# Performance work log

Hardware: AMD Instinct MI355X
Metric: run time of the kernel (lower is better)

The kernel has to match this reference:

```python
import jax, jax.numpy as jnp
import numpy as np

B, C_IN, H, W = 4, 256, 48, 48
HEADS, HD = 8, 64
N = H * W
SCALE = 1.0 / (HD ** 0.5)


def setup_inputs() -> dict:
    key = jax.random.key(0)
    ks = jax.random.split(key, 5)
    x = jax.random.normal(ks[0], (B, C_IN, H, W), dtype=jnp.float32)
    # 1x1 conv weights, squeezed: [heads, head_channels, in_channels]
    Wq = jax.random.normal(ks[1], (HEADS, HD, C_IN), dtype=jnp.float32) * (C_IN ** -0.5)
    Wk = jax.random.normal(ks[2], (HEADS, HD, C_IN), dtype=jnp.float32) * (C_IN ** -0.5)
    Wv = jax.random.normal(ks[3], (HEADS, HD, C_IN), dtype=jnp.float32) * (C_IN ** -0.5)
    # output 1x1 conv: [in_channels, heads*head_channels]
    Wo = jax.random.normal(ks[4], (C_IN, HEADS * HD), dtype=jnp.float32) * ((HEADS * HD) ** -0.5)
    return {"x": x, "Wq": Wq, "Wk": Wk, "Wv": Wv, "Wo": Wo}


def reference(x, Wq, Wk, Wv, Wo):
    b, c, h, w = x.shape
    n = h * w
    xf = x.reshape(b, c, n)  # [B, C, N]
    # per-head 1x1 convs == batched projections -> [heads, B, N, HD]
    q = jnp.einsum('hdc,bcn->hbnd', Wq, xf)
    k = jnp.einsum('hdc,bcn->hbnd', Wk, xf)
    v = jnp.einsum('hdc,bcn->hbnd', Wv, xf)
    scores = jnp.einsum('hbnd,hbmd->hbnm', q, k) * SCALE  # [heads, B, N, N]
    probs = jax.nn.softmax(scores, axis=-1)
    ws = jnp.einsum('hbnm,hbmd->hbnd', probs, v)  # [heads, B, N, HD]
    # faithful replication of torch: transpose(1,2) then reshape(B, heads*HD, H, W)
    ws = jnp.transpose(ws, (0, 2, 1, 3))  # [heads, N, B, HD]
    ws = ws.reshape(b, HEADS * HD, h, w)
    out = jnp.einsum('oc,bchw->bohw', Wo, ws)  # output 1x1 conv
    return out
```

## Files before the change

kernel.cpp:

```cpp
#include <hip/hip_runtime.h>

#define B_     4
#define CIN    256
#define NTOK   2304
#define HEADS  8
#define HD     64
#define SCALE  0.125f
#define LOG2E  1.44269504088896f
#define QSCALE (SCALE * LOG2E)
#define PBIAS  4.0f
#define QKV_ELEMS (HEADS * B_ * NTOK * HD)
#define HBSTRIDE 147456
#define WSZ    131072

typedef _Float16 f16;
typedef _Float16 __attribute__((ext_vector_type(8))) h8v;
typedef _Float16 __attribute__((ext_vector_type(4))) h4v;
typedef ushort   __attribute__((ext_vector_type(8))) us8;
typedef float    __attribute__((ext_vector_type(16))) f16v;

__device__ inline uint pk2(float a, float b) {
    auto v = __builtin_amdgcn_cvt_pkrtz(a, b);
    return __builtin_bit_cast(uint, v);
}
#define EXP2(x) __builtin_amdgcn_exp2f(x)

#define GLOAD_LDS(g, l) __builtin_amdgcn_global_load_lds( \
    (const __attribute__((address_space(1))) unsigned int*)(g), \
    (__attribute__((address_space(3))) unsigned int*)(l), 16, 0, 0)

__global__ __launch_bounds__(256) void castw(
    const float* __restrict__ Wq, const float* __restrict__ Wk,
    const float* __restrict__ Wv, const float* __restrict__ Wo,
    f16* __restrict__ wc, f16* __restrict__ woc)
{
    int e4 = (blockIdx.x * 256 + threadIdx.x) * 4;
    const float* src; f16* dst; float mult = 1.0f; int off;
    if (e4 < WSZ)          { src = Wq; off = e4;           dst = wc;           mult = QSCALE; }
    else if (e4 < 2 * WSZ) { src = Wk; off = e4 - WSZ;     dst = wc + WSZ; }
    else if (e4 < 3 * WSZ) { src = Wv; off = e4 - 2 * WSZ; dst = wc + 2 * WSZ; }
    else                   { src = Wo; off = e4 - 3 * WSZ; dst = woc; }
    float4 r = *(const float4*)(src + off);
    h4v hv;
    hv.x = (f16)(r.x * mult); hv.y = (f16)(r.y * mult);
    hv.z = (f16)(r.z * mult); hv.w = (f16)(r.w * mult);
    *(h4v*)(dst + off) = hv;
}

__global__ __launch_bounds__(256) void tcastf(
    const float* __restrict__ src, f16* __restrict__ dst, int C)
{
    const int n0 = blockIdx.x * 64;
    const int c0 = blockIdx.y * 64;
    const int b  = blockIdx.z;
    __shared__ float T[64][65];
    const int tid = threadIdx.x;
    const float* sb = src + ((size_t)b * C + c0) * NTOK;
    #pragma unroll
    for (int i = 0; i < 16; ++i) {
        int idx = tid + 256 * i;
        int rr = idx >> 6, ll = idx & 63;
        T[ll][rr] = sb[(size_t)rr * NTOK + n0 + ll];
    }
    __syncthreads();
    const size_t ob = ((size_t)b * NTOK + n0) * C + c0;
    #pragma unroll
    for (int i = 0; i < 4; ++i) {
        int idx = tid + 256 * i;
        int row = idx >> 4, c4 = (idx & 15) * 4;
        h4v v;
        v.x = (f16)T[row][c4 + 0]; v.y = (f16)T[row][c4 + 1];
        v.z = (f16)T[row][c4 + 2]; v.w = (f16)T[row][c4 + 3];
        *(h4v*)(dst + ob + (size_t)row * C + c4) = v;
    }
}

__global__ __launch_bounds__(128) void proj_mfma(
    const f16* __restrict__ wc, const f16* __restrict__ xt,
    f16* __restrict__ qh, f16* __restrict__ kh, f16* __restrict__ vth)
{
    const int ntile = blockIdx.x;
    const int hp    = blockIdx.y;
    const int b     = blockIdx.z;
    const int p     = hp >> 3, h = hp & 7;
    const int hb    = h * 4 + b;
    const f16* Wp = wc + ((size_t)p * 8 + h) * (HD * CIN);

    __shared__ __align__(16) f16 Ws[2][64][64], Xs[2][64][64];

    const int tid = threadIdx.x;
    const int w = tid >> 6, lane = tid & 63;
    const int lm = lane & 31, lh = lane >> 5;
    const int n_loc  = w * 32 + lm;
    const int n_glob = ntile * 64 + n_loc;

    const f16* xb = xt + ((size_t)b * NTOK + ntile * 64) * CIN;

    auto stage = [&](int buf, int c0) {
        const f16* src = (w == 0) ? Wp : xb;
        f16* dst = (w == 0) ? &Ws[buf][0][0] : &Xs[buf][0][0];
        #pragma unroll
        for (int i = 0; i < 8; ++i) {
            int g = i * 64 + lane; int row = g >> 3; int c = (g & 7) ^ (row & 7);
            GLOAD_LDS(src + (size_t)row * CIN + c0 + c * 8, dst + i * 512);
        }
    };

    f16v o0, o1;
    #pragma unroll
    for (int i = 0; i < 16; ++i) { o0[i] = 0.f; o1[i] = 0.f; }

    stage(0, 0);
    for (int c0 = 0; c0 < CIN; c0 += 64) {
        const int cur = (c0 >> 6) & 1;
        __syncthreads();
        if (c0 + 64 < CIN) stage(cur ^ 1, c0 + 64);
        #pragma unroll
        for (int s = 0; s < 4; ++s) {
            const int pp = ((2 * s + lh) ^ (lm & 7)) * 8;
            h8v a0 = *(const h8v*)&Ws[cur][lm][pp];
            h8v a1 = *(const h8v*)&Ws[cur][lm + 32][pp];
            h8v bh = *(const h8v*)&Xs[cur][n_loc][pp];
            o0 = __builtin_amdgcn_mfma_f32_32x32x16_f16(a0, bh, o0, 0, 0, 0);
            o1 = __builtin_amdgcn_mfma_f32_32x32x16_f16(a1, bh, o1, 0, 0, 0);
        }
    }

    const size_t hboff = (size_t)hb * HBSTRIDE;
    if (p < 2) {
        f16* oh = ((p == 0) ? qh : kh) + hboff + (size_t)n_glob * 64;
        #pragma unroll
        for (int t = 0; t < 2; ++t) {
            const f16v& oc = t ? o1 : o0;
            #pragma unroll
            for (int g = 0; g < 4; ++g) {
                int d0 = 8 * g + 4 * lh + 32 * t;
                h4v hv;
                hv.x = (f16)oc[4 * g + 0]; hv.y = (f16)oc[4 * g + 1];
                hv.z = (f16)oc[4 * g + 2]; hv.w = (f16)oc[4 * g + 3];
                *(h4v*)(oh + d0) = hv;
            }
        }
    } else {
        f16* oh = vth + hboff;
        #pragma unroll
        for (int t = 0; t < 2; ++t) {
            const f16v& oc = t ? o1 : o0;
            #pragma unroll
            for (int r = 0; r < 16; ++r) {
                int d = (r & 3) + 8 * (r >> 2) + 4 * lh + 32 * t;
                oh[(size_t)d * NTOK + n_glob] = (f16)oc[r];
            }
        }
    }
}

__global__ __launch_bounds__(256, 2) void attn_mfma(
    const f16* __restrict__ qh, const f16* __restrict__ kh,
    const f16* __restrict__ vth, f16* __restrict__ wsth)
{
    const int bid   = blockIdx.x;
    const int xcd   = bid & 7;
    const int slot  = bid >> 3;
    const int hb    = xcd * 4 + (slot / 18);
    const int rpair = slot % 18;
    const int h_    = hb >> 2, b = hb & 3;
    const int tid   = threadIdx.x;
    const int w     = tid >> 6;
    const int lane  = tid & 63;
    const int lm    = lane & 31;
    const int lh    = lane >> 5;
    const int qg    = w >> 1;
    const int ks    = w & 1;

    __shared__ __align__(16) f16 SMEM[2][2][2][64][64];

    const size_t hboff = (size_t)hb * HBSTRIDE;
    const int mA = rpair * 128 + qg * 64 + lm;
    const int mB = mA + 32;

    h8v QfA[4], QfB[4];
    #pragma unroll
    for (int s = 0; s < 4; ++s) {
        QfA[s] = *(const h8v*)(qh + hboff + (size_t)mA * 64 + (2 * s + lh) * 8);
        QfB[s] = *(const h8v*)(qh + hboff + (size_t)mB * 64 + (2 * s + lh) * 8);
    }

    f16v oA0, oA1, oB0, oB1;
    #pragma unroll
    for (int i = 0; i < 16; ++i) { oA0[i] = 0.f; oA1[i] = 0.f; oB0[i] = 0.f; oB1[i] = 0.f; }
    float lsumA = 0.f, lsumB = 0.f;

    const int  sv  = w >> 1;
    const int  stp = w & 1;
    const f16* gb  = (sv == 0) ? kh + hboff : vth + hboff;

    auto stage = [&](int buf, int st) {
        const int kts = 2 * st + stp;
        f16* dst = &SMEM[buf][sv][stp][0][0];
        #pragma unroll
        for (int i = 0; i < 8; ++i) {
            int g   = i * 64 + lane;
            int row = g >> 3;
            int c   = (g & 7) ^ (row & 7);
            const f16* src = (sv == 0)
                ? gb + kts * 4096 + row * 64 + c * 8
                : gb + (size_t)row * 2304 + kts * 64 + c * 8;
            GLOAD_LDS(src, dst + i * 512);
        }
    };

    stage(0, 0);
    __syncthreads();

    for (int st = 0; st < 18; ++st) {
        const int cur = st & 1;
        if (st + 1 < 18) stage(cur ^ 1, st + 1);

        f16v sA0, sA1, sB0, sB1;
        #pragma unroll
        for (int i = 0; i < 16; ++i) {
            sA0[i] = -PBIAS; sA1[i] = -PBIAS; sB0[i] = -PBIAS; sB1[i] = -PBIAS;
        }

        __builtin_amdgcn_s_setprio(1);
        #pragma unroll
        for (int s = 0; s < 4; ++s) {
            const int p = ((2 * s + lh) ^ (lm & 7)) * 8;
            h8v k0 = *(const h8v*)&SMEM[cur][0][ks][lm][p];
            h8v k1 = *(const h8v*)&SMEM[cur][0][ks][lm + 32][p];
            sA0 = __builtin_amdgcn_mfma_f32_32x32x16_f16(k0, QfA[s], sA0, 0, 0, 0);
            sA1 = __builtin_amdgcn_mfma_f32_32x32x16_f16(k1, QfA[s], sA1, 0, 0, 0);
            sB0 = __builtin_amdgcn_mfma_f32_32x32x16_f16(k0, QfB[s], sB0, 0, 0, 0);
            sB1 = __builtin_amdgcn_mfma_f32_32x32x16_f16(k1, QfB[s], sB1, 0, 0, 0);
        }
        __builtin_amdgcn_s_setprio(0);

        float rsA = 0.f, rsB = 0.f;
        #pragma unroll
        for (int i = 0; i < 16; ++i) { sA0[i] = EXP2(sA0[i]); rsA += sA0[i]; }
        #pragma unroll
        for (int i = 0; i < 16; ++i) { sA1[i] = EXP2(sA1[i]); rsA += sA1[i]; }
        #pragma unroll
        for (int i = 0; i < 16; ++i) { sB0[i] = EXP2(sB0[i]); rsB += sB0[i]; }
        #pragma unroll
        for (int i = 0; i < 16; ++i) { sB1[i] = EXP2(sB1[i]); rsB += sB1[i]; }
        lsumA += rsA; lsumB += rsB;

        uint PpkA[2][8], PpkB[2][8];
        #pragma unroll
        for (int pr = 0; pr < 8; ++pr) {
            PpkA[0][pr] = pk2(sA0[2 * pr], sA0[2 * pr + 1]);
            PpkA[1][pr] = pk2(sA1[2 * pr], sA1[2 * pr + 1]);
            PpkB[0][pr] = pk2(sB0[2 * pr], sB0[2 * pr + 1]);
            PpkB[1][pr] = pk2(sB1[2 * pr], sB1[2 * pr + 1]);
        }

        h8v pfA[4], pfB[4];
        #pragma unroll
        for (int s = 0; s < 4; ++s) {
            const int jt = s >> 1, q = 4 * (s & 1);
            auto a02 = __builtin_amdgcn_permlane32_swap(
                PpkA[jt][q + 0], PpkA[jt][q + 2], false, false);
            auto a13 = __builtin_amdgcn_permlane32_swap(
                PpkA[jt][q + 1], PpkA[jt][q + 3], false, false);
            uint4 ua = { a02[0], a13[0], a02[1], a13[1] };
            pfA[s] = __builtin_bit_cast(h8v, ua);
            auto b02 = __builtin_amdgcn_permlane32_swap(
                PpkB[jt][q + 0], PpkB[jt][q + 2], false, false);
            auto b13 = __builtin_amdgcn_permlane32_swap(
                PpkB[jt][q + 1], PpkB[jt][q + 3], false, false);
            uint4 ub = { b02[0], b13[0], b02[1], b13[1] };
            pfB[s] = __builtin_bit_cast(h8v, ub);
        }

        __builtin_amdgcn_s_setprio(1);
        #pragma unroll
        for (int s = 0; s < 4; ++s) {
            const int p = ((2 * s + lh) ^ (lm & 7)) * 8;
            h8v v0 = *(const h8v*)&SMEM[cur][1][ks][lm][p];
            h8v v1 = *(const h8v*)&SMEM[cur][1][ks][lm + 32][p];
            oA0 = __builtin_amdgcn_mfma_f32_32x32x16_f16(v0, pfA[s], oA0, 0, 0, 0);
            oA1 = __builtin_amdgcn_mfma_f32_32x32x16_f16(v1, pfA[s], oA1, 0, 0, 0);
            oB0 = __builtin_amdgcn_mfma_f32_32x32x16_f16(v0, pfB[s], oB0, 0, 0, 0);
            oB1 = __builtin_amdgcn_mfma_f32_32x32x16_f16(v1, pfB[s], oB1, 0, 0, 0);
        }
        __builtin_amdgcn_s_setprio(0);

        __syncthreads();
    }

    float* red = (float*)&SMEM[0][0][0][0][0];
    if (ks == 1) {
        float* dA = red + (size_t)(qg * 128 + lane) * 33;
        float* dB = red + (size_t)(qg * 128 + 64 + lane) * 33;
        #pragma unroll
        for (int i = 0; i < 16; ++i) {
            dA[i] = oA0[i]; dA[16 + i] = oA1[i];
            dB[i] = oB0[i]; dB[16 + i] = oB1[i];
        }
        dA[32] = lsumA; dB[32] = lsumB;
    }
    __syncthreads();
    if (ks == 0) {
        const float* sA = red + (size_t)(qg * 128 + lane) * 33;
        const float* sB = red + (size_t)(qg * 128 + 64 + lane) * 33;
        #pragma unroll
        for (int i = 0; i < 16; ++i) {
            oA0[i] += sA[i]; oA1[i] += sA[16 + i];
            oB0[i] += sB[i]; oB1[i] += sB[16 + i];
        }
        lsumA += sA[32]; lsumB += sB[32];
        lsumA += __shfl_xor(lsumA, 32);
        lsumB += __shfl_xor(lsumB, 32);
        float invA = 1.0f / lsumA, invB = 1.0f / lsumB;

        f16* wrA = wsth + ((size_t)h_ * NTOK + mA) * 256 + b * 64;
        f16* wrB = wsth + ((size_t)h_ * NTOK + mB) * 256 + b * 64;
        #pragma unroll
        for (int g = 0; g < 4; ++g) {
            h4v r0, r1;
            r0.x = (f16)(oA0[4 * g + 0] * invA); r0.y = (f16)(oA0[4 * g + 1] * invA);
            r0.z = (f16)(oA0[4 * g + 2] * invA); r0.w = (f16)(oA0[4 * g + 3] * invA);
            *(h4v*)(wrA + 8 * g + 4 * lh) = r0;
            r1.x = (f16)(oA1[4 * g + 0] * invA); r1.y = (f16)(oA1[4 * g + 1] * invA);
            r1.z = (f16)(oA1[4 * g + 2] * invA); r1.w = (f16)(oA1[4 * g + 3] * invA);
            *(h4v*)(wrA + 32 + 8 * g + 4 * lh) = r1;
        }
        #pragma unroll
        for (int g = 0; g < 4; ++g) {
            h4v r0, r1;
            r0.x = (f16)(oB0[4 * g + 0] * invB); r0.y = (f16)(oB0[4 * g + 1] * invB);
            r0.z = (f16)(oB0[4 * g + 2] * invB); r0.w = (f16)(oB0[4 * g + 3] * invB);
            *(h4v*)(wrB + 8 * g + 4 * lh) = r0;
            r1.x = (f16)(oB1[4 * g + 0] * invB); r1.y = (f16)(oB1[4 * g + 1] * invB);
            r1.z = (f16)(oB1[4 * g + 2] * invB); r1.w = (f16)(oB1[4 * g + 3] * invB);
            *(h4v*)(wrB + 32 + 8 * g + 4 * lh) = r1;
        }
    }
}

__global__ __launch_bounds__(128) void outconv_mfma(
    const f16* __restrict__ woc, const f16* __restrict__ ws,
    float* __restrict__ out)
{
    const int ntile = blockIdx.x;
    const int otile = blockIdx.y;
    const int b     = blockIdx.z;

    __shared__ __align__(16) f16 Wos[2][64][64];
    __shared__ __align__(16) f16 Xs[2][64][72];

    const int tid = threadIdx.x;
    const int w = tid >> 6, lane = tid & 63;
    const int lm = lane & 31, lh = lane >> 5;
    const int n_loc  = w * 32 + lm;
    const int n_glob = ntile * 64 + n_loc;
    const int pr = tid >> 2;
    const int qn = tid & 3;

    const f16* Wb = woc + (size_t)(otile * 64) * 512;
    const f16* wsb = ws + (size_t)b * 512 * NTOK + ntile * 64 + qn * 16;

    auto stageW = [&](int buf, int c0) {
        #pragma unroll
        for (int j = 0; j < 4; ++j) {
            int i = w * 4 + j;
            int g = i * 64 + lane; int row = g >> 3; int c = (g & 7) ^ (row & 7);
            GLOAD_LDS(Wb + (size_t)row * 512 + c0 + c * 8,
                      &Wos[buf][0][0] + i * 512);
        }
    };

    uint4 x0, x1, x2, x3;
    auto loadB = [&](int c0) {
        const f16* r0 = wsb + (size_t)(c0 + 2 * pr) * NTOK;
        const f16* r1 = r0 + NTOK;
        x0 = *(const uint4*)(r0);
        x1 = *(const uint4*)(r0 + 8);
        x2 = *(const uint4*)(r1);
        x3 = *(const uint4*)(r1 + 8);
    };
    auto storeB = [&](int buf) {
        us8 a0 = __builtin_bit_cast(us8, x0), a1 = __builtin_bit_cast(us8, x1);
        us8 b0 = __builtin_bit_cast(us8, x2), b1 = __builtin_bit_cast(us8, x3);
        #pragma unroll
        for (int j = 0; j < 8; ++j) {
            *(uint*)&Xs[buf][qn * 16 + j][2 * pr]     = (uint)a0[j] | ((uint)b0[j] << 16);
            *(uint*)&Xs[buf][qn * 16 + 8 + j][2 * pr] = (uint)a1[j] | ((uint)b1[j] << 16);
        }
    };

    f16v o0, o1;
    #pragma unroll
    for (int i = 0; i < 16; ++i) { o0[i] = 0.f; o1[i] = 0.f; }

    stageW(0, 0);
    loadB(0);
    storeB(0);
    for (int c0 = 0; c0 < 512; c0 += 64) {
        const int cur = (c0 >> 6) & 1;
        __syncthreads();
        if (c0 + 64 < 512) { stageW(cur ^ 1, c0 + 64); loadB(c0 + 64); }
        #pragma unroll
        for (int s = 0; s < 4; ++s) {
            const int pp = ((2 * s + lh) ^ (lm & 7)) * 8;
            const int co = (2 * s + lh) * 8;
            h8v a0 = *(const h8v*)&Wos[cur][lm][pp];
            h8v a1 = *(const h8v*)&Wos[cur][lm + 32][pp];
            h8v bh = *(const h8v*)&Xs[cur][n_loc][co];
            o0 = __builtin_amdgcn_mfma_f32_32x32x16_f16(a0, bh, o0, 0, 0, 0);
            o1 = __builtin_amdgcn_mfma_f32_32x32x16_f16(a1, bh, o1, 0, 0, 0);
        }
        if (c0 + 64 < 512) storeB(cur ^ 1);
    }

    #pragma unroll
    for (int t = 0; t < 2; ++t) {
        const f16v& oc = t ? o1 : o0;
        #pragma unroll
        for (int r = 0; r < 16; ++r) {
            int orow = otile * 64 + (r & 3) + 8 * (r >> 2) + 4 * lh + 32 * t;
            out[((size_t)b * CIN + orow) * NTOK + n_glob] = oc[r];
        }
    }
}

extern "C" void kernel_launch(void* const* d_in, const int* in_sizes, int n_in,
                              void* d_out, int out_size, void* d_ws, size_t ws_size,
                              hipStream_t stream)
{
    const float* x  = (const float*)d_in[0];
    const float* Wq = (const float*)d_in[1];
    const float* Wk = (const float*)d_in[2];
    const float* Wv = (const float*)d_in[3];
    const float* Wo = (const float*)d_in[4];
    float* out = (float*)d_out;

    f16* qh   = (f16*)d_ws;
    f16* kh   = qh   + QKV_ELEMS;
    f16* vth  = kh   + QKV_ELEMS;
    f16* wsth = vth  + QKV_ELEMS;
    f16* xt   = wsth;
    f16* wc   = wsth + QKV_ELEMS;
    f16* woc  = wc   + 3 * WSZ;

    castw<<<dim3(512), 256, 0, stream>>>(Wq, Wk, Wv, Wo, wc, woc);
    tcastf<<<dim3(36, 4, 4), 256, 0, stream>>>(x, xt, CIN);
    proj_mfma<<<dim3(36, 24, 4), 128, 0, stream>>>(wc, xt, qh, kh, vth);
    attn_mfma<<<dim3(576), 256, 0, stream>>>(qh, kh, vth, wsth);
    outconv_mfma<<<dim3(36, 4, 4), 128, 0, stream>>>(woc, wsth, out);
}
```

Baseline: 172.6 us.

## Drop key-split in attention and merge weight/input cast kernels into one launch

The attention kernel previously used four waves per block, two query groups times two key splits, and reduced partial outputs through LDS at the end. It now uses two waves per block, each owning a 64-row query tile and walking all 36 key tiles, with one wave staging K and the other V. This removes the cross-wave reduction and halves LDS per block. The cost is half as many waves per block and a longer serial loop per wave, which may reduce latency hiding. Separately, the weight-cast and input-transpose kernels are fused into one launch to save a kernel dispatch.

```diff
diff --git a/kernel.cpp b/kernel.cpp
--- a/kernel.cpp
+++ b/kernel.cpp
@@ -29,33 +29,36 @@
     (const __attribute__((address_space(1))) unsigned int*)(g), \
     (__attribute__((address_space(3))) unsigned int*)(l), 16, 0, 0)
 
-__global__ __launch_bounds__(256) void castw(
+__global__ __launch_bounds__(256) void prep(
+    const float* __restrict__ x,
     const float* __restrict__ Wq, const float* __restrict__ Wk,
     const float* __restrict__ Wv, const float* __restrict__ Wo,
-    f16* __restrict__ wc, f16* __restrict__ woc)
+    f16* __restrict__ wc, f16* __restrict__ woc, f16* __restrict__ xt)
 {
-    int e4 = (blockIdx.x * 256 + threadIdx.x) * 4;
-    const float* src; f16* dst; float mult = 1.0f; int off;
-    if (e4 < WSZ)          { src = Wq; off = e4;           dst = wc;           mult = QSCALE; }
-    else if (e4 < 2 * WSZ) { src = Wk; off = e4 - WSZ;     dst = wc + WSZ; }
-    else if (e4 < 3 * WSZ) { src = Wv; off = e4 - 2 * WSZ; dst = wc + 2 * WSZ; }
-    else                   { src = Wo; off = e4 - 3 * WSZ; dst = woc; }
-    float4 r = *(const float4*)(src + off);
-    h4v hv;
-    hv.x = (f16)(r.x * mult); hv.y = (f16)(r.y * mult);
-    hv.z = (f16)(r.z * mult); hv.w = (f16)(r.w * mult);
-    *(h4v*)(dst + off) = hv;
-}
-
-__global__ __launch_bounds__(256) void tcastf(
-    const float* __restrict__ src, f16* __restrict__ dst, int C)
-{
-    const int n0 = blockIdx.x * 64;
-    const int c0 = blockIdx.y * 64;
-    const int b  = blockIdx.z;
     __shared__ float T[64][65];
+    const int bid = blockIdx.x;
     const int tid = threadIdx.x;
-    const float* sb = src + ((size_t)b * C + c0) * NTOK;
+
+    if (bid < 512) {
+        int e4 = (bid * 256 + tid) * 4;
+        const float* src; f16* dst; float mult = 1.0f; int off;
+        if (e4 < WSZ)          { src = Wq; off = e4;           dst = wc;           mult = QSCALE; }
+        else if (e4 < 2 * WSZ) { src = Wk; off = e4 - WSZ;     dst = wc + WSZ; }
+        else if (e4 < 3 * WSZ) { src = Wv; off = e4 - 2 * WSZ; dst = wc + 2 * WSZ; }
+        else                   { src = Wo; off = e4 - 3 * WSZ; dst = woc; }
+        float4 r = *(const float4*)(src + off);
+        h4v hv;
+        hv.x = (f16)(r.x * mult); hv.y = (f16)(r.y * mult);
+        hv.z = (f16)(r.z * mult); hv.w = (f16)(r.w * mult);
+        *(h4v*)(dst + off) = hv;
+        return;
+    }
+
+    const int r  = bid - 512;
+    const int n0 = (r % 36) * 64;
+    const int c0 = ((r / 36) % 4) * 64;
+    const int b  = r / 144;
+    const float* sb = x + ((size_t)b * CIN + c0) * NTOK;
     #pragma unroll
     for (int i = 0; i < 16; ++i) {
         int idx = tid + 256 * i;
@@ -63,7 +66,7 @@
         T[ll][rr] = sb[(size_t)rr * NTOK + n0 + ll];
     }
     __syncthreads();
-    const size_t ob = ((size_t)b * NTOK + n0) * C + c0;
+    const size_t ob = ((size_t)b * NTOK + n0) * CIN + c0;
     #pragma unroll
     for (int i = 0; i < 4; ++i) {
         int idx = tid + 256 * i;
@@ -71,7 +74,7 @@
         h4v v;
         v.x = (f16)T[row][c4 + 0]; v.y = (f16)T[row][c4 + 1];
         v.z = (f16)T[row][c4 + 2]; v.w = (f16)T[row][c4 + 3];
-        *(h4v*)(dst + ob + (size_t)row * C + c4) = v;
+        *(h4v*)(xt + ob + (size_t)row * CIN + c4) = v;
     }
 }
 
@@ -155,7 +158,7 @@
     }
 }
 
-__global__ __launch_bounds__(256, 2) void attn_mfma(
+__global__ __launch_bounds__(128, 2) void attn_mfma(
     const f16* __restrict__ qh, const f16* __restrict__ kh,
     const f16* __restrict__ vth, f16* __restrict__ wsth)
 {
@@ -163,20 +166,18 @@
     const int xcd   = bid & 7;
     const int slot  = bid >> 3;
     const int hb    = xcd * 4 + (slot / 18);
-    const int rpair = slot % 18;
+    const int rtile = slot % 18;
     const int h_    = hb >> 2, b = hb & 3;
     const int tid   = threadIdx.x;
     const int w     = tid >> 6;
     const int lane  = tid & 63;
     const int lm    = lane & 31;
     const int lh    = lane >> 5;
-    const int qg    = w >> 1;
-    const int ks    = w & 1;
-
-    __shared__ __align__(16) f16 SMEM[2][2][2][64][64];
+
+    __shared__ __align__(16) f16 SMEM[2][2][64][64];
 
     const size_t hboff = (size_t)hb * HBSTRIDE;
-    const int mA = rpair * 128 + qg * 64 + lm;
+    const int mA = rtile * 128 + w * 64 + lm;
     const int mB = mA + 32;
 
     h8v QfA[4], QfB[4];
@@ -191,21 +192,18 @@
     for (int i = 0; i < 16; ++i) { oA0[i] = 0.f; oA1[i] = 0.f; oB0[i] = 0.f; oB1[i] = 0.f; }
     float lsumA = 0.f, lsumB = 0.f;
 
-    const int  sv  = w >> 1;
-    const int  stp = w & 1;
-    const f16* gb  = (sv == 0) ? kh + hboff : vth + hboff;
-
-    auto stage = [&](int buf, int st) {
-        const int kts = 2 * st + stp;
-        f16* dst = &SMEM[buf][sv][stp][0][0];
+    const f16* gb = (w == 0) ? kh + hboff : vth + hboff;
+
+    auto stage = [&](int buf, int kt) {
+        f16* dst = &SMEM[buf][w][0][0];
         #pragma unroll
         for (int i = 0; i < 8; ++i) {
             int g   = i * 64 + lane;
             int row = g >> 3;
             int c   = (g & 7) ^ (row & 7);
-            const f16* src = (sv == 0)
-                ? gb + kts * 4096 + row * 64 + c * 8
-                : gb + (size_t)row * 2304 + kts * 64 + c * 8;
+            const f16* src = (w == 0)
+                ? gb + kt * 4096 + row * 64 + c * 8
+                : gb + (size_t)row * 2304 + kt * 64 + c * 8;
             GLOAD_LDS(src, dst + i * 512);
         }
     };
@@ -213,9 +211,9 @@
     stage(0, 0);
     __syncthreads();
 
-    for (int st = 0; st < 18; ++st) {
-        const int cur = st & 1;
-        if (st + 1 < 18) stage(cur ^ 1, st + 1);
+    for (int kt = 0; kt < 36; ++kt) {
+        const int cur = kt & 1;
+        if (kt + 1 < 36) stage(cur ^ 1, kt + 1);
 
         f16v sA0, sA1, sB0, sB1;
         #pragma unroll
@@ -227,8 +225,8 @@
         #pragma unroll
         for (int s = 0; s < 4; ++s) {
             const int p = ((2 * s + lh) ^ (lm & 7)) * 8;
-            h8v k0 = *(const h8v*)&SMEM[cur][0][ks][lm][p];
-            h8v k1 = *(const h8v*)&SMEM[cur][0][ks][lm + 32][p];
+            h8v k0 = *(const h8v*)&SMEM[cur][0][lm][p];
+            h8v k1 = *(const h8v*)&SMEM[cur][0][lm + 32][p];
             sA0 = __builtin_amdgcn_mfma_f32_32x32x16_f16(k0, QfA[s], sA0, 0, 0, 0);
             sA1 = __builtin_amdgcn_mfma_f32_32x32x16_f16(k1, QfA[s], sA1, 0, 0, 0);
             sB0 = __builtin_amdgcn_mfma_f32_32x32x16_f16(k0, QfB[s], sB0, 0, 0, 0);
@@ -278,8 +276,8 @@
         #pragma unroll
         for (int s = 0; s < 4; ++s) {
             const int p = ((2 * s + lh) ^ (lm & 7)) * 8;
-            h8v v0 = *(const h8v*)&SMEM[cur][1][ks][lm][p];
-            h8v v1 = *(const h8v*)&SMEM[cur][1][ks][lm + 32][p];
+            h8v v0 = *(const h8v*)&SMEM[cur][1][lm][p];
+            h8v v1 = *(const h8v*)&SMEM[cur][1][lm + 32][p];
             oA0 = __builtin_amdgcn_mfma_f32_32x32x16_f16(v0, pfA[s], oA0, 0, 0, 0);
             oA1 = __builtin_amdgcn_mfma_f32_32x32x16_f16(v1, pfA[s], oA1, 0, 0, 0);
             oB0 = __builtin_amdgcn_mfma_f32_32x32x16_f16(v0, pfB[s], oB0, 0, 0, 0);
@@ -290,53 +288,31 @@
         __syncthreads();
     }
 
-    float* red = (float*)&SMEM[0][0][0][0][0];
-    if (ks == 1) {
-        float* dA = red + (size_t)(qg * 128 + lane) * 33;
-        float* dB = red + (size_t)(qg * 128 + 64 + lane) * 33;
-        #pragma unroll
-        for (int i = 0; i < 16; ++i) {
-            dA[i] = oA0[i]; dA[16 + i] = oA1[i];
-            dB[i] = oB0[i]; dB[16 + i] = oB1[i];
-        }
-        dA[32] = lsumA; dB[32] = lsumB;
-    }
-    __syncthreads();
-    if (ks == 0) {
-        const float* sA = red + (size_t)(qg * 128 + lane) * 33;
-        const float* sB = red + (size_t)(qg * 128 + 64 + lane) * 33;
-        #pragma unroll
-        for (int i = 0; i < 16; ++i) {
-            oA0[i] += sA[i]; oA1[i] += sA[16 + i];
-            oB0[i] += sB[i]; oB1[i] += sB[16 + i];
-        }
-        lsumA += sA[32]; lsumB += sB[32];
-        lsumA += __shfl_xor(lsumA, 32);
-        lsumB += __shfl_xor(lsumB, 32);
-        float invA = 1.0f / lsumA, invB = 1.0f / lsumB;
-
-        f16* wrA = wsth + ((size_t)h_ * NTOK + mA) * 256 + b * 64;
-        f16* wrB = wsth + ((size_t)h_ * NTOK + mB) * 256 + b * 64;
-        #pragma unroll
-        for (int g = 0; g < 4; ++g) {
-            h4v r0, r1;
-            r0.x = (f16)(oA0[4 * g + 0] * invA); r0.y = (f16)(oA0[4 * g + 1] * invA);
-            r0.z = (f16)(oA0[4 * g + 2] * invA); r0.w = (f16)(oA0[4 * g + 3] * invA);
-            *(h4v*)(wrA + 8 * g + 4 * lh) = r0;
-            r1.x = (f16)(oA1[4 * g + 0] * invA); r1.y = (f16)(oA1[4 * g + 1] * invA);
-            r1.z = (f16)(oA1[4 * g + 2] * invA); r1.w = (f16)(oA1[4 * g + 3] * invA);
-            *(h4v*)(wrA + 32 + 8 * g + 4 * lh) = r1;
-        }
-        #pragma unroll
-        for (int g = 0; g < 4; ++g) {
-            h4v r0, r1;
-            r0.x = (f16)(oB0[4 * g + 0] * invB); r0.y = (f16)(oB0[4 * g + 1] * invB);
-            r0.z = (f16)(oB0[4 * g + 2] * invB); r0.w = (f16)(oB0[4 * g + 3] * invB);
-            *(h4v*)(wrB + 8 * g + 4 * lh) = r0;
-            r1.x = (f16)(oB1[4 * g + 0] * invB); r1.y = (f16)(oB1[4 * g + 1] * invB);
-            r1.z = (f16)(oB1[4 * g + 2] * invB); r1.w = (f16)(oB1[4 * g + 3] * invB);
-            *(h4v*)(wrB + 32 + 8 * g + 4 * lh) = r1;
-        }
+    lsumA += __shfl_xor(lsumA, 32);
+    lsumB += __shfl_xor(lsumB, 32);
+    float invA = 1.0f / lsumA, invB = 1.0f / lsumB;
+
+    f16* wrA = wsth + ((size_t)h_ * NTOK + mA) * 256 + b * 64;
+    f16* wrB = wsth + ((size_t)h_ * NTOK + mB) * 256 + b * 64;
+    #pragma unroll
+    for (int g = 0; g < 4; ++g) {
+        h4v r0, r1;
+        r0.x = (f16)(oA0[4 * g + 0] * invA); r0.y = (f16)(oA0[4 * g + 1] * invA);
+        r0.z = (f16)(oA0[4 * g + 2] * invA); r0.w = (f16)(oA0[4 * g + 3] * invA);
+        *(h4v*)(wrA + 8 * g + 4 * lh) = r0;
+        r1.x = (f16)(oA1[4 * g + 0] * invA); r1.y = (f16)(oA1[4 * g + 1] * invA);
+        r1.z = (f16)(oA1[4 * g + 2] * invA); r1.w = (f16)(oA1[4 * g + 3] * invA);
+        *(h4v*)(wrA + 32 + 8 * g + 4 * lh) = r1;
+    }
+    #pragma unroll
+    for (int g = 0; g < 4; ++g) {
+        h4v r0, r1;
+        r0.x = (f16)(oB0[4 * g + 0] * invB); r0.y = (f16)(oB0[4 * g + 1] * invB);
+        r0.z = (f16)(oB0[4 * g + 2] * invB); r0.w = (f16)(oB0[4 * g + 3] * invB);
+        *(h4v*)(wrB + 8 * g + 4 * lh) = r0;
+        r1.x = (f16)(oB1[4 * g + 0] * invB); r1.y = (f16)(oB1[4 * g + 1] * invB);
+        r1.z = (f16)(oB1[4 * g + 2] * invB); r1.w = (f16)(oB1[4 * g + 3] * invB);
+        *(h4v*)(wrB + 32 + 8 * g + 4 * lh) = r1;
     }
 }
 
@@ -445,9 +421,8 @@
     f16* wc   = wsth + QKV_ELEMS;
     f16* woc  = wc   + 3 * WSZ;
 
-    castw<<<dim3(512), 256, 0, stream>>>(Wq, Wk, Wv, Wo, wc, woc);
-    tcastf<<<dim3(36, 4, 4), 256, 0, stream>>>(x, xt, CIN);
+    prep<<<dim3(1088), 256, 0, stream>>>(x, Wq, Wk, Wv, Wo, wc, woc, xt);
     proj_mfma<<<dim3(36, 24, 4), 128, 0, stream>>>(wc, xt, qh, kh, vth);
-    attn_mfma<<<dim3(576), 256, 0, stream>>>(qh, kh, vth, wsth);
+    attn_mfma<<<dim3(576), 128, 0, stream>>>(qh, kh, vth, wsth);
     outconv_mfma<<<dim3(36, 4, 4), 128, 0, stream>>>(woc, wsth, out);
 }
```

After: 178.9 us. +3.7%, slower.
